# Kernel optimization log

Hardware: AMD Instinct MI355X
Metric: run time of the kernel (lower is better)

Reference implementation:

```python
import jax, jax.numpy as jnp
import numpy as np

N_HYP = 128           # HPARAM.HV_NUM_OF_HYPOTHESES
ZSCORE_THR = 2.0      # HPARAM.PRUN_ZSCORE_THRESHOLD
IN_MASK_MULT = 10.0   # HPARAM.HV_HYPOTHESIS_IN_MASK_MULTIPLIER


def setup_inputs() -> dict:
    key = jax.random.key(0)
    k1, k2 = jax.random.split(key)
    B, H, W = 16, 96, 96
    uv_img = jax.random.normal(k1, (B, 2, H, W), dtype=jnp.float32)
    mask = jnp.ones((B, H, W), dtype=bool)  # all-ones mask: pts == full pixel grid
    # stands in for torch.multinomial pair sampling over mask pixels
    pair_idx = jax.random.randint(k2, (B, N_HYP, 2), 0, H * W)
    return {"uv_img": uv_img, "mask": mask, "pair_idx": pair_idx}


def _hough_voting(uv_img, pair_idx):
    B, _, H, W = uv_img.shape
    Np = H * W
    # pts in torch.where(mask) row-major order for an all-ones mask
    ys, xs = jnp.meshgrid(jnp.arange(H), jnp.arange(W), indexing='ij')
    pts = jnp.stack([ys.ravel(), xs.ravel()], axis=1).astype(uv_img.dtype)  # [Np,2]
    uvT = uv_img.reshape(B, 2, Np).transpose(0, 2, 1)                       # [B,Np,2]

    # --- hypothesis generation (pair gather + batched 2x2 pinverse solve) ---
    pp = pts[pair_idx]                                   # [B,N,2(pair),2(yx)]
    p0, p1 = pp[:, :, 0], pp[:, :, 1]                    # [B,N,2]
    uv0 = jnp.take_along_axis(uvT, pair_idx[:, :, 0][:, :, None], axis=1)  # [B,N,2]
    uv1 = jnp.take_along_axis(uvT, pair_idx[:, :, 1][:, :, None], axis=1)  # [B,N,2]
    A = jnp.stack([uv0, -uv1], axis=-1)                  # [B,N,2,2]
    Bvec = (p1 - p0)[..., None]                          # [B,N,2,1]
    X = jnp.linalg.pinv(A) @ Bvec                        # [B,N,2,1]
    s = X[:, :, 0, :]                                    # [B,N,1] scale along ray 0
    Y = s * uv0 + p0                                     # [B,N,2] intersection points

    # --- z-score outlier pruning with mean replacement ---
    mean = jnp.mean(Y, axis=1)                           # [B,2]
    std = jnp.std(Y, axis=1, ddof=1)                     # torch.std is unbiased
    z = (Y - mean[:, None, :]) / std[:, None, :]
    outl = (z > ZSCORE_THR)
    outl = (outl[..., 0] | outl[..., 1])[..., None]
    Yp = jnp.where(outl, mean[:, None, :], Y)

    # --- pairwise vote weighting over all mask pixels ---
    a = Yp[:, :, None, :] - pts[None, None]              # [B,N,Np,2]
    a = a / jnp.linalg.norm(a, axis=-1, keepdims=True)
    votes = jnp.einsum('bnpk,bpk->bnp', a, uvT) > 0      # direction agreement
    w = jnp.sum(votes, axis=-1).astype(uv_img.dtype)     # [B,N]
    match = jnp.trunc(Yp)[:, :, None, :] == pts[None, None]
    h_in_mask = jnp.sum(match[..., 0] & match[..., 1], axis=-1)
    w = jnp.where(h_in_mask == 1, IN_MASK_MULT, 1.0) * w
    w = w / jnp.sum(w, axis=1, keepdims=True)

    # --- NaN guard + weighted mean, swap (y,x)->(x,y) ---
    is_nan = jnp.isnan(Yp[..., 0]) | jnp.isnan(Yp[..., 1])
    Yp = jnp.nan_to_num(Yp)
    w = jnp.where(is_nan, 0.0, w)
    weighted_mean = jnp.sum(Yp * w[..., None], axis=1)   # [B,2]
    return weighted_mean[:, ::-1]


def reference(uv_img, mask, pair_idx):
    # mask is all-ones by construction; pts are the full pixel grid (see _hough_voting)
    return _hough_voting(uv_img, pair_idx)
```

## Files before the change

### kernel.cpp

```cpp
#include <hip/hip_runtime.h>
#include <math.h>

namespace {

constexpr int BATCH = 16;
constexpr int Ww = 96;
constexpr int NP = 96 * 96;
constexpr int NHYP = 128;
constexpr int HPB = 2;
constexpr int GPB = NHYP / HPB;

__device__ inline void waveSum2D(double& a, double& b) {
#pragma unroll
  for (int o = 32; o >= 1; o >>= 1) {
    a += __shfl_xor(a, o, 64);
    b += __shfl_xor(b, o, 64);
  }
}
__device__ inline void waveSum2I(int& a, int& b) {
#pragma unroll
  for (int o = 32; o >= 1; o >>= 1) {
    a += __shfl_xor(a, o, 64);
    b += __shfl_xor(b, o, 64);
  }
}
__device__ inline double waveSumD(double v) {
#pragma unroll
  for (int o = 32; o >= 1; o >>= 1) v += __shfl_xor(v, o, 64);
  return v;
}

__global__ __launch_bounds__(256, 4)
void vote_kernel(const float* __restrict__ uv, const int* __restrict__ pair,
                 double* __restrict__ partials ) {
  __shared__ double sPy[NHYP], sPx[NHYP];
  __shared__ float sWm[NHYP];
  __shared__ int sNan[NHYP];
  __shared__ double sh[2][2];
  __shared__ int sC[4][2];

  const int t = threadIdx.x;
  const int lane = t & 63;
  const int wv = t >> 6;
  const int b = blockIdx.x >> 6;
  const int g = blockIdx.x & (GPB - 1);
  const float* uvb = uv + (size_t)b * 2 * NP;

  double Yy = 0.0, Yx = 0.0;
  if (t < NHYP) {
    int i0 = pair[(b * NHYP + t) * 2 + 0];
    int i1 = pair[(b * NHYP + t) * 2 + 1];
    double u0 = uvb[i0], v0 = uvb[NP + i0];
    double u1 = uvb[i1], v1 = uvb[NP + i1];
    double y0 = (double)(i0 / Ww), x0 = (double)(i0 % Ww);
    double y1 = (double)(i1 / Ww), x1 = (double)(i1 % Ww);
    double det = u1 * v0 - u0 * v1;
    double s = (u1 * (x1 - x0) - v1 * (y1 - y0)) / det;
    Yy = s * u0 + y0;
    Yx = s * v0 + x0;
  }
  double sy = Yy, sx = Yx;
  waveSum2D(sy, sx);
  if (lane == 0 && wv < 2) { sh[wv][0] = sy; sh[wv][1] = sx; }
  __syncthreads();
  const double my = (sh[0][0] + sh[1][0]) * (1.0 / NHYP);
  const double mx = (sh[0][1] + sh[1][1]) * (1.0 / NHYP);
  const double dy = Yy - my, dx = Yx - mx;
  double qy = dy * dy, qx = dx * dx;
  waveSum2D(qy, qx);
  __syncthreads();
  if (lane == 0 && wv < 2) { sh[wv][0] = qy; sh[wv][1] = qx; }
  __syncthreads();
  if (t < NHYP) {
    double vy = (sh[0][0] + sh[1][0]) * (1.0 / (NHYP - 1));
    double vx = (sh[0][1] + sh[1][1]) * (1.0 / (NHYP - 1));
    bool outl = (dy > 2.0 * sqrt(vy)) || (dx > 2.0 * sqrt(vx));
    double py = outl ? my : Yy;
    double px = outl ? mx : Yx;
    sPy[t] = py;
    sPx[t] = px;
    sWm[t] = (py > -1.0 && py < 96.0 && px > -1.0 && px < 96.0) ? 10.0f : 1.0f;
    sNan[t] = (isnan(py) || isnan(px)) ? 1 : 0;
  }
  __syncthreads();

  const int h0 = g * HPB, h1 = h0 + 1;
  const float yy0 = (float)sPy[h0], yx0 = (float)sPx[h0];
  const float yy1 = (float)sPy[h1], yx1 = (float)sPx[h1];
  int c0 = 0, c1 = 0;
#pragma unroll
  for (int it = 0; it < 9; ++it) {
    const int p = (it * 256 + t) * 4;
    const float4 u4 = *(const float4*)(uvb + p);
    const float4 v4 = *(const float4*)(uvb + NP + p);
    const int yi = p / Ww;
    const float fy = (float)yi;
    const float fx = (float)(p - yi * Ww);
    const float k0 = fy * u4.x + fx * v4.x;
    const float k1 = fy * u4.y + (fx + 1.0f) * v4.y;
    const float k2 = fy * u4.z + (fx + 2.0f) * v4.z;
    const float k3 = fy * u4.w + (fx + 3.0f) * v4.w;
    c0 += (fmaf(yy0, u4.x, yx0 * v4.x) > k0) ? 1 : 0;
    c0 += (fmaf(yy0, u4.y, yx0 * v4.y) > k1) ? 1 : 0;
    c0 += (fmaf(yy0, u4.z, yx0 * v4.z) > k2) ? 1 : 0;
    c0 += (fmaf(yy0, u4.w, yx0 * v4.w) > k3) ? 1 : 0;
    c1 += (fmaf(yy1, u4.x, yx1 * v4.x) > k0) ? 1 : 0;
    c1 += (fmaf(yy1, u4.y, yx1 * v4.y) > k1) ? 1 : 0;
    c1 += (fmaf(yy1, u4.z, yx1 * v4.z) > k2) ? 1 : 0;
    c1 += (fmaf(yy1, u4.w, yx1 * v4.w) > k3) ? 1 : 0;
  }
  waveSum2I(c0, c1);
  if (lane == 0) { sC[wv][0] = c0; sC[wv][1] = c1; }
  __syncthreads();

  if (t == 0) {
    int cnt0 = sC[0][0] + sC[1][0] + sC[2][0] + sC[3][0];
    int cnt1 = sC[0][1] + sC[1][1] + sC[2][1] + sC[3][1];
    double w0 = sNan[h0] ? 0.0 : (double)cnt0 * (double)sWm[h0];
    double w1 = sNan[h1] ? 0.0 : (double)cnt1 * (double)sWm[h1];
    double ny = (sNan[h0] ? 0.0 : sPy[h0] * w0) +
                (sNan[h1] ? 0.0 : sPy[h1] * w1);
    double nx = (sNan[h0] ? 0.0 : sPx[h0] * w0) +
                (sNan[h1] ? 0.0 : sPx[h1] * w1);
    double* slot = partials + (size_t)b * 3 * GPB;
    slot[0 * GPB + g] = w0 + w1;
    slot[1 * GPB + g] = ny;
    slot[2 * GPB + g] = nx;
  }
}

__global__ __launch_bounds__(192)
void final_kernel(const double* __restrict__ partials,
                  float* __restrict__ out) {
  __shared__ double sD[3];
  const int t = threadIdx.x;
  const int lane = t & 63;
  const int wv = t >> 6;
  const int b = blockIdx.x;

  double val = partials[((size_t)b * 3 + wv) * GPB + lane];
  val = waveSumD(val);
  if (lane == 0) sD[wv] = val;
  __syncthreads();
  if (t == 0) {
    double wsum = sD[0];
    out[b * 2 + 0] = (float)(sD[2] / wsum);
    out[b * 2 + 1] = (float)(sD[1] / wsum);
  }
}

}

extern "C" void kernel_launch(void* const* d_in, const int* in_sizes, int n_in,
                              void* d_out, int out_size, void* d_ws, size_t ws_size,
                              hipStream_t stream) {
  const float* uv = (const float*)d_in[0];
  const int* pair = (const int*)d_in[2];
  float* out = (float*)d_out;

  double* partials = (double*)d_ws;

  vote_kernel<<<BATCH * GPB, 256, 0, stream>>>(uv, pair, partials);
  final_kernel<<<BATCH, 192, 0, stream>>>(partials, out);
}
```

Before: 15.09 us.

## Process four hypotheses per block, prefetch uv before solve, count votes via ballot

Raises hypotheses per block from two to four, which halves the block count and makes each pixel load serve more hypotheses. The first three uv tiles are loaded into registers before the hypothesis solve so their latency overlaps that prologue. Per-lane vote counters and the final shuffle reduction are replaced by ballot plus popcount, and one barrier is dropped by using separate shared buffers for the two reductions. Fewer blocks means less parallelism across the GPU, and the extra prefetch registers raise register pressure.

```diff
diff --git a/kernel.cpp b/kernel.cpp
--- a/kernel.cpp
+++ b/kernel.cpp
@@ -7,17 +7,10 @@
 constexpr int Ww = 96;
 constexpr int NP = 96 * 96;
 constexpr int NHYP = 128;
-constexpr int HPB = 2;
+constexpr int HPB = 4;
 constexpr int GPB = NHYP / HPB;
 
 __device__ inline void waveSum2D(double& a, double& b) {
-#pragma unroll
-  for (int o = 32; o >= 1; o >>= 1) {
-    a += __shfl_xor(a, o, 64);
-    b += __shfl_xor(b, o, 64);
-  }
-}
-__device__ inline void waveSum2I(int& a, int& b) {
 #pragma unroll
   for (int o = 32; o >= 1; o >>= 1) {
     a += __shfl_xor(a, o, 64);
@@ -36,15 +29,23 @@
   __shared__ double sPy[NHYP], sPx[NHYP];
   __shared__ float sWm[NHYP];
   __shared__ int sNan[NHYP];
-  __shared__ double sh[2][2];
-  __shared__ int sC[4][2];
+  __shared__ double sh1[2][2], sh2[2][2];
+  __shared__ unsigned sC[4][HPB];
 
   const int t = threadIdx.x;
   const int lane = t & 63;
   const int wv = t >> 6;
-  const int b = blockIdx.x >> 6;
+  const int b = blockIdx.x >> 5;
   const int g = blockIdx.x & (GPB - 1);
   const float* uvb = uv + (size_t)b * 2 * NP;
+
+  float4 pu[3], pv[3];
+#pragma unroll
+  for (int i = 0; i < 3; ++i) {
+    const int p = (i * 256 + t) * 4;
+    pu[i] = *(const float4*)(uvb + p);
+    pv[i] = *(const float4*)(uvb + NP + p);
+  }
 
   double Yy = 0.0, Yx = 0.0;
   if (t < NHYP) {
@@ -61,19 +62,18 @@
   }
   double sy = Yy, sx = Yx;
   waveSum2D(sy, sx);
-  if (lane == 0 && wv < 2) { sh[wv][0] = sy; sh[wv][1] = sx; }
+  if (lane == 0 && wv < 2) { sh1[wv][0] = sy; sh1[wv][1] = sx; }
   __syncthreads();
-  const double my = (sh[0][0] + sh[1][0]) * (1.0 / NHYP);
-  const double mx = (sh[0][1] + sh[1][1]) * (1.0 / NHYP);
+  const double my = (sh1[0][0] + sh1[1][0]) * (1.0 / NHYP);
+  const double mx = (sh1[0][1] + sh1[1][1]) * (1.0 / NHYP);
   const double dy = Yy - my, dx = Yx - mx;
   double qy = dy * dy, qx = dx * dx;
   waveSum2D(qy, qx);
-  __syncthreads();
-  if (lane == 0 && wv < 2) { sh[wv][0] = qy; sh[wv][1] = qx; }
+  if (lane == 0 && wv < 2) { sh2[wv][0] = qy; sh2[wv][1] = qx; }
   __syncthreads();
   if (t < NHYP) {
-    double vy = (sh[0][0] + sh[1][0]) * (1.0 / (NHYP - 1));
-    double vx = (sh[0][1] + sh[1][1]) * (1.0 / (NHYP - 1));
+    double vy = (sh2[0][0] + sh2[1][0]) * (1.0 / (NHYP - 1));
+    double vx = (sh2[0][1] + sh2[1][1]) * (1.0 / (NHYP - 1));
     bool outl = (dy > 2.0 * sqrt(vy)) || (dx > 2.0 * sqrt(vx));
     double py = outl ? my : Yy;
     double px = outl ? mx : Yx;
@@ -84,15 +84,25 @@
   }
   __syncthreads();
 
-  const int h0 = g * HPB, h1 = h0 + 1;
-  const float yy0 = (float)sPy[h0], yx0 = (float)sPx[h0];
-  const float yy1 = (float)sPy[h1], yx1 = (float)sPx[h1];
-  int c0 = 0, c1 = 0;
+  const int hb = g * HPB;
+  float yy[HPB], yx[HPB];
+#pragma unroll
+  for (int h = 0; h < HPB; ++h) {
+    yy[h] = (float)sPy[hb + h];
+    yx[h] = (float)sPx[hb + h];
+  }
+  unsigned c[HPB] = {0, 0, 0, 0};
 #pragma unroll
   for (int it = 0; it < 9; ++it) {
+    float4 u4, v4;
+    if (it < 3) {
+      u4 = pu[it]; v4 = pv[it];
+    } else {
+      const int p = (it * 256 + t) * 4;
+      u4 = *(const float4*)(uvb + p);
+      v4 = *(const float4*)(uvb + NP + p);
+    }
     const int p = (it * 256 + t) * 4;
-    const float4 u4 = *(const float4*)(uvb + p);
-    const float4 v4 = *(const float4*)(uvb + NP + p);
     const int yi = p / Ww;
     const float fy = (float)yi;
     const float fx = (float)(p - yi * Ww);
@@ -100,30 +110,35 @@
     const float k1 = fy * u4.y + (fx + 1.0f) * v4.y;
     const float k2 = fy * u4.z + (fx + 2.0f) * v4.z;
     const float k3 = fy * u4.w + (fx + 3.0f) * v4.w;
-    c0 += (fmaf(yy0, u4.x, yx0 * v4.x) > k0) ? 1 : 0;
-    c0 += (fmaf(yy0, u4.y, yx0 * v4.y) > k1) ? 1 : 0;
-    c0 += (fmaf(yy0, u4.z, yx0 * v4.z) > k2) ? 1 : 0;
-    c0 += (fmaf(yy0, u4.w, yx0 * v4.w) > k3) ? 1 : 0;
-    c1 += (fmaf(yy1, u4.x, yx1 * v4.x) > k0) ? 1 : 0;
-    c1 += (fmaf(yy1, u4.y, yx1 * v4.y) > k1) ? 1 : 0;
-    c1 += (fmaf(yy1, u4.z, yx1 * v4.z) > k2) ? 1 : 0;
-    c1 += (fmaf(yy1, u4.w, yx1 * v4.w) > k3) ? 1 : 0;
+#pragma unroll
+    for (int h = 0; h < HPB; ++h) {
+      c[h] += __popcll(__ballot(fmaf(yy[h], u4.x, yx[h] * v4.x) > k0));
+      c[h] += __popcll(__ballot(fmaf(yy[h], u4.y, yx[h] * v4.y) > k1));
+      c[h] += __popcll(__ballot(fmaf(yy[h], u4.z, yx[h] * v4.z) > k2));
+      c[h] += __popcll(__ballot(fmaf(yy[h], u4.w, yx[h] * v4.w) > k3));
+    }
   }
-  waveSum2I(c0, c1);
-  if (lane == 0) { sC[wv][0] = c0; sC[wv][1] = c1; }
+  if (lane == 0) {
+#pragma unroll
+    for (int h = 0; h < HPB; ++h) sC[wv][h] = c[h];
+  }
   __syncthreads();
 
   if (t == 0) {
-    int cnt0 = sC[0][0] + sC[1][0] + sC[2][0] + sC[3][0];
-    int cnt1 = sC[0][1] + sC[1][1] + sC[2][1] + sC[3][1];
-    double w0 = sNan[h0] ? 0.0 : (double)cnt0 * (double)sWm[h0];
-    double w1 = sNan[h1] ? 0.0 : (double)cnt1 * (double)sWm[h1];
-    double ny = (sNan[h0] ? 0.0 : sPy[h0] * w0) +
-                (sNan[h1] ? 0.0 : sPy[h1] * w1);
-    double nx = (sNan[h0] ? 0.0 : sPx[h0] * w0) +
-                (sNan[h1] ? 0.0 : sPx[h1] * w1);
+    double wsum = 0.0, ny = 0.0, nx = 0.0;
+#pragma unroll
+    for (int h = 0; h < HPB; ++h) {
+      const int hh = hb + h;
+      unsigned cnt = sC[0][h] + sC[1][h] + sC[2][h] + sC[3][h];
+      if (!sNan[hh]) {
+        double w = (double)cnt * (double)sWm[hh];
+        wsum += w;
+        ny += sPy[hh] * w;
+        nx += sPx[hh] * w;
+      }
+    }
     double* slot = partials + (size_t)b * 3 * GPB;
-    slot[0 * GPB + g] = w0 + w1;
+    slot[0 * GPB + g] = wsum;
     slot[1 * GPB + g] = ny;
     slot[2 * GPB + g] = nx;
   }
@@ -138,7 +153,9 @@
   const int wv = t >> 6;
   const int b = blockIdx.x;
 
-  double val = partials[((size_t)b * 3 + wv) * GPB + lane];
+  double val = (lane < GPB)
+                   ? partials[((size_t)b * 3 + wv) * GPB + lane]
+                   : 0.0;
   val = waveSumD(val);
   if (lane == 0) sD[wv] = val;
   __syncthreads();
```

Measured after the change: 17.10 us. 13.3% more time.
